# Optimization experiments

Hardware: AMD Instinct MI355X
Metric: run time of the kernel (lower is better)

The kernel has to match this reference:

```python
import jax, jax.numpy as jnp
import numpy as np

N = 200_000      # nodes
E = 6_400_000    # edges (avg degree 32)
ATT = 16         # scorer hidden dim
MAXD = 512       # mixer max_depth
C = 1.0          # curvature
EPS = 1e-15


def _mobius_add(a, b, c):
    # Mobius addition on the Poincare ball: a (+)_c b
    ab = jnp.sum(a * b, axis=-1, keepdims=True)
    aa = jnp.sum(a * a, axis=-1, keepdims=True)
    bb = jnp.sum(b * b, axis=-1, keepdims=True)
    num = (1.0 + 2.0 * c * ab + c * bb) * a + (1.0 - c * aa) * b
    den = 1.0 + 2.0 * c * ab + (c * c) * aa * bb
    return num / jnp.maximum(den, EPS)


def setup_inputs() -> dict:
    key = jax.random.key(0)
    ks = jax.random.split(key, 8)
    x = jax.random.normal(ks[0], (N, 2), dtype=jnp.float32)
    # keep nodes strictly inside the unit Poincare disk (|x| < 0.5)
    x = 0.5 * x / (1.0 + jnp.linalg.norm(x, axis=-1, keepdims=True))
    edge_index = jax.random.randint(ks[1], (2, E), 0, N, dtype=jnp.int32)
    depth = jax.random.randint(ks[2], (N,), 0, MAXD, dtype=jnp.int32)
    W1 = jax.random.normal(ks[3], (2, ATT), dtype=jnp.float32) * (1.0 / np.sqrt(2.0))
    b1 = jnp.zeros((ATT,), dtype=jnp.float32)
    W2 = jax.random.normal(ks[4], (ATT, 1), dtype=jnp.float32) * (1.0 / np.sqrt(ATT))
    eta = jnp.array(1.0, dtype=jnp.float32)
    depth_scale = 1.0 + 0.1 * jax.random.normal(ks[5], (MAXD, 1), dtype=jnp.float32)
    depth_theta = 0.1 * jax.random.normal(ks[6], (MAXD, 1), dtype=jnp.float32)
    return dict(x=x, edge_index=edge_index, depth=depth, W1=W1, b1=b1, W2=W2,
                eta=eta, depth_scale=depth_scale, depth_theta=depth_theta)


def reference(x, edge_index, depth, W1, b1, W2, eta, depth_scale, depth_theta):
    c = C
    sc = jnp.sqrt(jnp.asarray(c, dtype=x.dtype))
    row, col = edge_index[0], edge_index[1]
    xi = x[row]   # [E,2] target node of each edge
    xj = x[col]   # [E,2] source node of each edge

    # log_{xi}(xj): tangent vector at xi
    u = _mobius_add(-xi, xj, c)                                        # [E,2]
    un = jnp.maximum(jnp.linalg.norm(u, axis=-1, keepdims=True), EPS)  # [E,1]
    lam_i = 2.0 / jnp.maximum(1.0 - c * jnp.sum(xi * xi, axis=-1, keepdims=True), EPS)
    v = (2.0 / (sc * lam_i)) * jnp.arctanh(jnp.minimum(sc * un, 1.0 - 1e-5)) * (u / un)

    # tiny MLP attention score per edge
    h = jax.nn.gelu(v @ W1 + b1, approximate=False)   # [E,ATT]
    scores = (h @ W2)[:, 0]                           # [E]

    # segment softmax over edges grouped by target node `row`
    smax = jax.ops.segment_max(scores, row, num_segments=N)
    ex = jnp.exp(scores - smax[row])
    denom = jax.ops.segment_sum(ex, row, num_segments=N)
    alpha = ex / jnp.maximum(denom[row], 1e-15)       # [E]

    # weighted scatter-add of tangent vectors
    m = jax.ops.segment_sum(alpha[:, None] * v, row, num_segments=N)   # [N,2]

    # depth-gated rotation/scale in the tangent space (mixer)
    d = jnp.clip(depth, 0, MAXD - 1)
    k = depth_scale[d]            # [N,1]
    ang = depth_theta[d][:, 0]    # [N]
    ca, sa = jnp.cos(ang), jnp.sin(ang)
    m = k * jnp.stack([ca * m[:, 0] - sa * m[:, 1],
                       sa * m[:, 0] + ca * m[:, 1]], axis=-1)

    # exp_{x}(eta * m)
    w = eta * m
    wn = jnp.maximum(jnp.linalg.norm(w, axis=-1, keepdims=True), EPS)
    lam_x = 2.0 / jnp.maximum(1.0 - c * jnp.sum(x * x, axis=-1, keepdims=True), EPS)
    second = jnp.tanh(sc * lam_x * wn / 2.0) * (w / (sc * wn))
    return _mobius_add(x, second, c)
```

## Files before the change

### kernel.cpp

```cpp
#include <hip/hip_runtime.h>
#include <hip/hip_fp16.h>
#include <math.h>

#define EPSF 1e-15f
#define BSH  8
#define BSZ  (1 << BSH)
#define BMSK (BSZ - 1)
#define CAPB 9216
#define MAXNB 1024
#define AGG_T 1024
#define BIN_T 1024
#define LCH   6400

#define TBL   128
#define TW    129
#define VMIN  (-1.2f)
#define VH    (2.4f / 128.0f)
#define INVH  (128.0f / 2.4f)

__device__ __forceinline__ float fast_rcp(float x)  { return __builtin_amdgcn_rcpf(x); }
__device__ __forceinline__ float fast_rsq(float x)  { return __builtin_amdgcn_rsqf(x); }
__device__ __forceinline__ float fast_exp(float x)  { return __builtin_amdgcn_exp2f(x * 1.4426950408889634f); }

__device__ __forceinline__ unsigned int float_to_ordered(float f) {
    unsigned int u = __float_as_uint(f);
    return (u & 0x80000000u) ? ~u : (u | 0x80000000u);
}
__device__ __forceinline__ float ordered_to_float(unsigned int u) {
    u = (u & 0x80000000u) ? (u & 0x7FFFFFFFu) : ~u;
    return __uint_as_float(u);
}

__device__ __forceinline__ void edge_v_fast(float2 xi, float2 xj, float& vx, float& vy) {
    float ab = -(xi.x * xj.x + xi.y * xj.y);
    float aa = xi.x * xi.x + xi.y * xi.y;
    float bb = xj.x * xj.x + xj.y * xj.y;
    float f1 = 1.0f + 2.0f * ab + bb;
    float f2 = 1.0f - aa;
    float ux = f1 * (-xi.x) + f2 * xj.x;
    float uy = f1 * (-xi.y) + f2 * xj.y;
    float den = 1.0f + 2.0f * ab + aa * bb;
    float inv_den = fast_rcp(fmaxf(den, EPSF));
    ux *= inv_den; uy *= inv_den;
    float un2 = fmaxf(ux * ux + uy * uy, 1e-24f);
    float inv_un = fast_rsq(un2);
    float un = fminf(un2 * inv_un, 1.0f - 1e-5f);
    float t = 0.34657359027997264f * __builtin_amdgcn_logf((1.0f + un) * fast_rcp(1.0f - un));
    float s = fmaxf(f2, EPSF) * t * inv_un;
    vx = s * ux; vy = s * uy;
}

__device__ __forceinline__ void edge_v(float2 xi, float2 xj, float& vx, float& vy) {
    float ab = -(xi.x * xj.x + xi.y * xj.y);
    float aa = xi.x * xi.x + xi.y * xi.y;
    float bb = xj.x * xj.x + xj.y * xj.y;
    float f1 = 1.0f + 2.0f * ab + bb;
    float f2 = 1.0f - aa;
    float ux = f1 * (-xi.x) + f2 * xj.x;
    float uy = f1 * (-xi.y) + f2 * xj.y;
    float den = 1.0f + 2.0f * ab + aa * bb;
    float inv_den = 1.0f / fmaxf(den, EPSF);
    ux *= inv_den; uy *= inv_den;
    float un = fmaxf(sqrtf(ux * ux + uy * uy), EPSF);
    float t  = atanhf(fminf(un, 1.0f - 1e-5f));
    float s = fmaxf(f2, EPSF) * t / un;
    vx = s * ux; vy = s * uy;
}

__device__ __forceinline__ float edge_score(float vx, float vy,
                                            const float* __restrict__ W1,
                                            const float* __restrict__ b1,
                                            const float* __restrict__ W2) {
    float score = 0.0f;
#pragma unroll
    for (int k = 0; k < 16; ++k) {
        float z = fmaf(vx, W1[k], fmaf(vy, W1[16 + k], b1[k]));
        float g = 0.5f * z * (1.0f + erff(z * 0.70710678118654752f));
        score = fmaf(g, W2[k], score);
    }
    return score;
}

__device__ __forceinline__ float2 finalize_node(float2 xv, float mx, float my,
                                                int d, float eta,
                                                const float* __restrict__ dscale,
                                                const float* __restrict__ dtheta) {
    d = d < 0 ? 0 : (d > 511 ? 511 : d);
    float k   = dscale[d];
    float ang = dtheta[d];
    float ca = cosf(ang), sa = sinf(ang);
    float m0 = k * (ca * mx - sa * my);
    float m1 = k * (sa * mx + ca * my);

    float wx = eta * m0, wy = eta * m1;
    float wn = fmaxf(sqrtf(wx * wx + wy * wy), 1e-15f);

    float aa = xv.x * xv.x + xv.y * xv.y;
    float lam = 2.0f / fmaxf(1.0f - aa, 1e-15f);
    float fac = tanhf(lam * wn * 0.5f) / wn;
    float sx = fac * wx, sy = fac * wy;

    float ab = xv.x * sx + xv.y * sy;
    float bb = sx * sx + sy * sy;
    float n1 = 1.0f + 2.0f * ab + bb;
    float n2 = 1.0f - aa;
    float ox = n1 * xv.x + n2 * sx;
    float oy = n1 * xv.y + n2 * sy;
    float dd = 1.0f + 2.0f * ab + aa * bb;
    float inv = 1.0f / fmaxf(dd, 1e-15f);
    return make_float2(ox * inv, oy * inv);
}


__global__ void init_cursor(unsigned* __restrict__ cursor, int NB) {
    int b = blockIdx.x * blockDim.x + threadIdx.x;
    if (b < NB) cursor[b] = (unsigned)b * CAPB;
}

__global__ void build_score_table(const float* __restrict__ W1,
                                  const float* __restrict__ b1,
                                  const float* __restrict__ W2,
                                  float* __restrict__ tbl) {
    int i = blockIdx.x * blockDim.x + threadIdx.x;
    if (i >= TW * TW) return;
    int iy = i / TW, ix = i - iy * TW;
    float vx = VMIN + VH * (float)ix;
    float vy = VMIN + VH * (float)iy;
    tbl[i] = edge_score(vx, vy, W1, b1, W2);
}

__global__ __launch_bounds__(BIN_T)
void bin_edges(const int* __restrict__ ei,
               unsigned* __restrict__ cursor,
               unsigned* __restrict__ sorted,
               int E, int NB) {
    __shared__ unsigned bkrank[LCH];
    __shared__ unsigned payload[LCH];
    __shared__ unsigned sortedLoc[LCH];
    __shared__ unsigned gdst[LCH];
    __shared__ unsigned hist[MAXNB];
    __shared__ unsigned scanA[MAXNB];
    __shared__ unsigned loc[MAXNB];
    __shared__ unsigned gbase[MAXNB];

    int tid = threadIdx.x;
    int e0 = blockIdx.x * LCH;
    int cnt = min(E - e0, LCH);
    if (cnt <= 0) return;

    if (tid < MAXNB) hist[tid] = 0;
    __syncthreads();

    for (int idx = tid; idx < cnt; idx += BIN_T) {
        int r = ei[e0 + idx];
        int c = ei[E + e0 + idx];
        unsigned bk = (unsigned)r >> BSH;
        unsigned rank = atomicAdd(&hist[bk], 1u);
        bkrank[idx] = (bk << 14) | rank;
        payload[idx] = ((unsigned)(r & BMSK) << 24) | (unsigned)c;
    }
    __syncthreads();

    unsigned h = (tid < MAXNB) ? hist[tid] : 0u;
    if (tid < MAXNB) scanA[tid] = h;
    __syncthreads();
#pragma unroll
    for (int step = 1; step < MAXNB; step <<= 1) {
        unsigned v = 0u;
        if (tid < MAXNB) {
            v = scanA[tid];
            if (tid >= step) v += scanA[tid - step];
        }
        __syncthreads();
        if (tid < MAXNB) scanA[tid] = v;
        __syncthreads();
    }
    if (tid < MAXNB) {
        loc[tid] = scanA[tid] - h;
        gbase[tid] = h ? atomicAdd(&cursor[tid], h) : 0u;
    }
    __syncthreads();

    for (int idx = tid; idx < cnt; idx += BIN_T) {
        unsigned v = bkrank[idx];
        unsigned bk = v >> 14;
        unsigned rank = v & 0x3FFFu;
        unsigned pos = loc[bk] + rank;
        sortedLoc[pos] = payload[idx];
        unsigned g = gbase[bk] + rank;
        gdst[pos] = (g < (bk + 1u) * CAPB) ? g : 0xFFFFFFFFu;
    }
    __syncthreads();

    for (int idx = tid; idx < cnt; idx += BIN_T) {
        unsigned g = gdst[idx];
        if (g != 0xFFFFFFFFu) sorted[g] = sortedLoc[idx];
    }
}

__global__ __launch_bounds__(AGG_T, 8)
void aggregate(const float2* __restrict__ x,
               const unsigned* __restrict__ cursor,
               const unsigned* __restrict__ sorted,
               const int* __restrict__ depth,
               const float* __restrict__ tbl,
               const float* __restrict__ etaPtr,
               const float* __restrict__ dscale,
               const float* __restrict__ dtheta,
               float2* __restrict__ out, int N) {
    __shared__ float2 xr[BSZ];
    __shared__ unsigned stashA[CAPB];
    __shared__ unsigned stashV[CAPB];
    __shared__ unsigned nmax[BSZ];
    __shared__ unsigned long long accP[BSZ];

    int b = blockIdx.x;
    int tid = threadIdx.x;
    int nb0 = b << BSH;
    int nodeCnt = min(BSZ, N - nb0);
    if (tid < BSZ) {
        nmax[tid] = 0u;
        accP[tid] = 0ull;
        if (tid < nodeCnt) xr[tid] = x[nb0 + tid];
    }
    __syncthreads();

    unsigned basep = (unsigned)b * CAPB;
    unsigned cnt = cursor[b] - basep;
    cnt = cnt > (unsigned)CAPB ? (unsigned)CAPB : cnt;

    for (unsigned i = tid; i < cnt; i += AGG_T) {
        unsigned u = sorted[basep + i];
        int rl = (int)(u >> 24);
        int c  = (int)(u & 0xFFFFFFu);
        float2 xi = xr[rl];
        float2 xj = x[c];
        float vx, vy;
        edge_v_fast(xi, xj, vx, vy);

        float tx = fminf(fmaxf((vx - VMIN) * INVH, 0.0f), 127.999f);
        float ty = fminf(fmaxf((vy - VMIN) * INVH, 0.0f), 127.999f);
        int ix = (int)tx, iy = (int)ty;
        float fx = tx - (float)ix, fy = ty - (float)iy;
        const float* row = tbl + iy * TW + ix;
        float s00 = row[0], s01 = row[1];
        float s10 = row[TW], s11 = row[TW + 1];
        float sA = fmaf(fx, s01 - s00, s00);
        float sB = fmaf(fx, s11 - s10, s10);
        float score = fmaf(fy, sB - sA, sA);

        __half hs = __float2half_rn(score);
        float sq = __half2float(hs);
        unsigned short s16 = *(unsigned short*)&hs;
        __half2 h2 = __floats2half2_rn(vx, vy);
        stashA[i] = ((unsigned)rl << 16) | (unsigned)s16;
        stashV[i] = *(unsigned*)&h2;
        atomicMax(&nmax[rl], float_to_ordered(sq));
    }
    __syncthreads();

    for (unsigned i = tid; i < cnt; i += AGG_T) {
        unsigned a = stashA[i];
        int rl = (int)(a >> 16);
        unsigned short s16 = (unsigned short)(a & 0xFFFFu);
        __half hs = *(__half*)&s16;
        float s = __half2float(hs);
        float mxs = ordered_to_float(nmax[rl]);
        float ex = fast_exp(s - mxs);
        unsigned vv = stashV[i];
        __half2 h2 = *(__half2*)&vv;
        float2 v2 = __half22float2(h2);
        unsigned e0 = __float2uint_rn(ex * 16384.0f);
        unsigned e1 = __float2uint_rn(ex * (v2.x + 2.0f) * 0.25f * 16384.0f);
        unsigned e2 = __float2uint_rn(ex * (v2.y + 2.0f) * 0.25f * 16384.0f);
        unsigned long long pk = (unsigned long long)e0
                              | ((unsigned long long)e1 << 21)
                              | ((unsigned long long)e2 << 42);
        atomicAdd(&accP[rl], pk);
    }
    __syncthreads();

    if (tid >= nodeCnt) return;
    unsigned long long w = accP[tid];
    float F0 = (float)(unsigned int)(w & 0x1FFFFFull);
    float F1 = (float)(unsigned int)((w >> 21) & 0x1FFFFFull);
    float F2 = (float)(unsigned int)(w >> 42);
    float mx = 0.0f, my = 0.0f;
    if (F0 > 0.0f) {
        float inv = 1.0f / F0;
        mx = 4.0f * F1 * inv - 2.0f;
        my = 4.0f * F2 * inv - 2.0f;
    }
    int i = nb0 + tid;
    out[i] = finalize_node(xr[tid], mx, my, depth[i], etaPtr[0], dscale, dtheta);
}


__global__ void init_kernel(unsigned int* __restrict__ smax,
                            unsigned long long* __restrict__ maccP, int N) {
    int i = blockIdx.x * blockDim.x + threadIdx.x;
    if (i < N) {
        smax[i] = float_to_ordered(-INFINITY);
        maccP[i] = 0ull;
    }
}

__global__ void pass1_score_max(const float2* __restrict__ x,
                                const int* __restrict__ ei,
                                const float* __restrict__ W1,
                                const float* __restrict__ b1,
                                const float* __restrict__ W2,
                                unsigned int* __restrict__ smax, int E) {
    int e = blockIdx.x * blockDim.x + threadIdx.x;
    if (e >= E) return;
    int r = ei[e];
    int c = ei[E + e];
    float vx, vy;
    edge_v(x[r], x[c], vx, vy);
    float score = edge_score(vx, vy, W1, b1, W2);
    atomicMax(&smax[r], float_to_ordered(score));
}

#define PK_SCALE 16384.0f

__global__ void pass2_accum(const float2* __restrict__ x,
                            const int* __restrict__ ei,
                            const float* __restrict__ W1,
                            const float* __restrict__ b1,
                            const float* __restrict__ W2,
                            const unsigned int* __restrict__ smax,
                            unsigned long long* __restrict__ maccP, int E) {
    int e = blockIdx.x * blockDim.x + threadIdx.x;
    if (e >= E) return;
    int r = ei[e];
    int c = ei[E + e];
    float vx, vy;
    edge_v(x[r], x[c], vx, vy);
    float score = edge_score(vx, vy, W1, b1, W2);
    float mx = ordered_to_float(smax[r]);
    float ex = expf(score - mx);
    unsigned e0 = __float2uint_rn(ex * PK_SCALE);
    unsigned e1 = __float2uint_rn(ex * (vx + 2.0f) * 0.25f * PK_SCALE);
    unsigned e2 = __float2uint_rn(ex * (vy + 2.0f) * 0.25f * PK_SCALE);
    unsigned long long pk = (unsigned long long)e0
                          | ((unsigned long long)e1 << 21)
                          | ((unsigned long long)e2 << 42);
    atomicAdd(&maccP[r], pk);
}

__global__ void pass3_finalize(const float2* __restrict__ x,
                               const int* __restrict__ depth,
                               const unsigned long long* __restrict__ maccP,
                               const float* __restrict__ etaPtr,
                               const float* __restrict__ dscale,
                               const float* __restrict__ dtheta,
                               float2* __restrict__ out, int N) {
    int i = blockIdx.x * blockDim.x + threadIdx.x;
    if (i >= N) return;
    unsigned long long w = maccP[i];
    float F0 = (float)(unsigned int)(w & 0x1FFFFFull);
    float F1 = (float)(unsigned int)((w >> 21) & 0x1FFFFFull);
    float F2 = (float)(unsigned int)(w >> 42);
    float mx = 0.0f, my = 0.0f;
    if (F0 > 0.0f) {
        float inv = 1.0f / F0;
        mx = 4.0f * F1 * inv - 2.0f;
        my = 4.0f * F2 * inv - 2.0f;
    }
    out[i] = finalize_node(x[i], mx, my, depth[i], etaPtr[0], dscale, dtheta);
}


extern "C" void kernel_launch(void* const* d_in, const int* in_sizes, int n_in,
                              void* d_out, int out_size, void* d_ws, size_t ws_size,
                              hipStream_t stream) {
    const float2* x   = (const float2*)d_in[0];
    const int* ei     = (const int*)d_in[1];
    const int* depth  = (const int*)d_in[2];
    const float* W1   = (const float*)d_in[3];
    const float* b1   = (const float*)d_in[4];
    const float* W2   = (const float*)d_in[5];
    const float* eta  = (const float*)d_in[6];
    const float* dsc  = (const float*)d_in[7];
    const float* dth  = (const float*)d_in[8];
    float2* out = (float2*)d_out;

    int N = in_sizes[0] / 2;
    int E = in_sizes[1] / 2;
    int NB = (N + BSZ - 1) >> BSH;

    const int B = 256;
    size_t sortedBytes = (size_t)NB * CAPB * 4;
    size_t need = 4096 + sortedBytes + (size_t)TW * TW * 4;
    if (NB <= MAXNB && ws_size >= need) {
        unsigned* cursor = (unsigned*)d_ws;
        unsigned* sorted = (unsigned*)((char*)d_ws + 4096);
        float* tbl = (float*)((char*)d_ws + 4096 + sortedBytes);
        int binG = (E + LCH - 1) / LCH;
        init_cursor<<<(NB + B - 1) / B, B, 0, stream>>>(cursor, NB);
        build_score_table<<<(TW * TW + B - 1) / B, B, 0, stream>>>(W1, b1, W2, tbl);
        bin_edges<<<binG, BIN_T, 0, stream>>>(ei, cursor, sorted, E, NB);
        aggregate<<<NB, AGG_T, 0, stream>>>(x, cursor, sorted, depth, tbl,
                                            eta, dsc, dth, out, N);
    } else {
        unsigned long long* maccP = (unsigned long long*)d_ws;
        unsigned int* smax = (unsigned int*)(maccP + N);
        init_kernel<<<(N + B - 1) / B, B, 0, stream>>>(smax, maccP, N);
        pass1_score_max<<<(E + B - 1) / B, B, 0, stream>>>(x, ei, W1, b1, W2, smax, E);
        pass2_accum<<<(E + B - 1) / B, B, 0, stream>>>(x, ei, W1, b1, W2, smax, maccP, E);
        pass3_finalize<<<(N + B - 1) / B, B, 0, stream>>>(x, depth, maccP, eta, dsc, dth, out, N);
    }
}
```

Baseline: 195.3 us.

## Keep per-edge stash in registers and batch-load edge gathers in aggregate

Replaces the two 9216-entry LDS stash arrays with per-thread register arrays covering a fixed 9 slots per thread. Each thread first issues all of its sorted-edge loads and then all of its x[c] gathers, so the gathers are in flight together rather than serialized with compute. Dropping about 72KB of LDS per block should allow more blocks per CU. The cost is higher register pressure from the fully unrolled loops, and inactive slots still read sorted and x[0].

```diff
diff --git a/kernel.cpp b/kernel.cpp
--- a/kernel.cpp
+++ b/kernel.cpp
@@ -9,6 +9,7 @@
 #define CAPB 9216
 #define MAXNB 1024
 #define AGG_T 1024
+#define KSL   9
 #define BIN_T 1024
 #define LCH   6400
 
@@ -209,8 +210,6 @@
                const float* __restrict__ dtheta,
                float2* __restrict__ out, int N) {
     __shared__ float2 xr[BSZ];
-    __shared__ unsigned stashA[CAPB];
-    __shared__ unsigned stashV[CAPB];
     __shared__ unsigned nmax[BSZ];
     __shared__ unsigned long long accP[BSZ];
 
@@ -228,15 +227,34 @@
     unsigned basep = (unsigned)b * CAPB;
     unsigned cnt = cursor[b] - basep;
     cnt = cnt > (unsigned)CAPB ? (unsigned)CAPB : cnt;
-
-    for (unsigned i = tid; i < cnt; i += AGG_T) {
-        unsigned u = sorted[basep + i];
-        int rl = (int)(u >> 24);
-        int c  = (int)(u & 0xFFFFFFu);
-        float2 xi = xr[rl];
-        float2 xj = x[c];
+    const unsigned* __restrict__ sb = sorted + basep;
+
+    unsigned u[KSL];
+#pragma unroll
+    for (int k = 0; k < KSL; ++k) {
+        u[k] = sb[(unsigned)tid + (unsigned)(k * AGG_T)];
+    }
+
+    int rl[KSL];
+    float2 xj[KSL];
+#pragma unroll
+    for (int k = 0; k < KSL; ++k) {
+        unsigned i = (unsigned)tid + (unsigned)(k * AGG_T);
+        bool act = i < cnt;
+        rl[k] = (int)(u[k] >> 24);
+        int c = act ? (int)(u[k] & 0xFFFFFFu) : 0;
+        xj[k] = x[c];
+    }
+
+    unsigned pkA[KSL];
+    unsigned pkV[KSL];
+#pragma unroll
+    for (int k = 0; k < KSL; ++k) {
+        unsigned i = (unsigned)tid + (unsigned)(k * AGG_T);
+        bool act = i < cnt;
+        float2 xi = xr[rl[k]];
         float vx, vy;
-        edge_v_fast(xi, xj, vx, vy);
+        edge_v_fast(xi, xj[k], vx, vy);
 
         float tx = fminf(fmaxf((vx - VMIN) * INVH, 0.0f), 127.999f);
         float ty = fminf(fmaxf((vy - VMIN) * INVH, 0.0f), 127.999f);
@@ -253,22 +271,23 @@
         float sq = __half2float(hs);
         unsigned short s16 = *(unsigned short*)&hs;
         __half2 h2 = __floats2half2_rn(vx, vy);
-        stashA[i] = ((unsigned)rl << 16) | (unsigned)s16;
-        stashV[i] = *(unsigned*)&h2;
-        atomicMax(&nmax[rl], float_to_ordered(sq));
-    }
-    __syncthreads();
-
-    for (unsigned i = tid; i < cnt; i += AGG_T) {
-        unsigned a = stashA[i];
-        int rl = (int)(a >> 16);
-        unsigned short s16 = (unsigned short)(a & 0xFFFFu);
+        pkA[k] = ((unsigned)rl[k] << 16) | (unsigned)s16;
+        pkV[k] = *(unsigned*)&h2;
+        if (act) atomicMax(&nmax[rl[k]], float_to_ordered(sq));
+    }
+    __syncthreads();
+
+#pragma unroll
+    for (int k = 0; k < KSL; ++k) {
+        unsigned i = (unsigned)tid + (unsigned)(k * AGG_T);
+        if (i >= cnt) continue;
+        int rlk = (int)(pkA[k] >> 16);
+        unsigned short s16 = (unsigned short)(pkA[k] & 0xFFFFu);
         __half hs = *(__half*)&s16;
         float s = __half2float(hs);
-        float mxs = ordered_to_float(nmax[rl]);
+        float mxs = ordered_to_float(nmax[rlk]);
         float ex = fast_exp(s - mxs);
-        unsigned vv = stashV[i];
-        __half2 h2 = *(__half2*)&vv;
+        __half2 h2 = *(__half2*)&pkV[k];
         float2 v2 = __half22float2(h2);
         unsigned e0 = __float2uint_rn(ex * 16384.0f);
         unsigned e1 = __float2uint_rn(ex * (v2.x + 2.0f) * 0.25f * 16384.0f);
@@ -276,7 +295,7 @@
         unsigned long long pk = (unsigned long long)e0
                               | ((unsigned long long)e1 << 21)
                               | ((unsigned long long)e2 << 42);
-        atomicAdd(&accP[rl], pk);
+        atomicAdd(&accP[rlk], pk);
     }
     __syncthreads();
 
```

Result: no change. 193.0 us (-1.2%).

## Replace edge binning with global-max softmax and direct global atomics

Applied to the files above, without the earlier changes.

Drops the bucket-sort and per-node segment max. The softmax is stabilised with the global maximum of the score lookup table, which is mathematically equivalent. Each edge then atomically adds fixed-point weighted sums straight into per-node global accumulators, with the table staged in LDS. This removes the bin_edges pass and the sorted buffer traffic, but adds 6.4M random global 64-bit and 32-bit atomics, and it risks fixed-point underflow when a node's scores sit far below the global max.

```diff
diff --git a/kernel.cpp b/kernel.cpp
--- a/kernel.cpp
+++ b/kernel.cpp
@@ -3,20 +3,19 @@
 #include <math.h>
 
 #define EPSF 1e-15f
-#define BSH  8
-#define BSZ  (1 << BSH)
-#define BMSK (BSZ - 1)
-#define CAPB 9216
-#define MAXNB 1024
-#define AGG_T 1024
-#define BIN_T 1024
-#define LCH   6400
 
 #define TBL   128
 #define TW    129
+#define TWSZ  (TW * TW)
+#define TW4   ((TWSZ) / 4)
 #define VMIN  (-1.2f)
 #define VH    (2.4f / 128.0f)
 #define INVH  (128.0f / 2.4f)
+
+#define ACC_SCALE 16777216.0f
+
+#define FUS_T 1024
+#define FPT   4
 
 __device__ __forceinline__ float fast_rcp(float x)  { return __builtin_amdgcn_rcpf(x); }
 __device__ __forceinline__ float fast_rsq(float x)  { return __builtin_amdgcn_rsqf(x); }
@@ -112,187 +111,124 @@
 }
 
 
-__global__ void init_cursor(unsigned* __restrict__ cursor, int NB) {
-    int b = blockIdx.x * blockDim.x + threadIdx.x;
-    if (b < NB) cursor[b] = (unsigned)b * CAPB;
-}
-
 __global__ void build_score_table(const float* __restrict__ W1,
                                   const float* __restrict__ b1,
                                   const float* __restrict__ W2,
-                                  float* __restrict__ tbl) {
+                                  float* __restrict__ tbl,
+                                  unsigned* __restrict__ tblMaxSlot) {
     int i = blockIdx.x * blockDim.x + threadIdx.x;
-    if (i >= TW * TW) return;
+    if (i >= TWSZ) return;
     int iy = i / TW, ix = i - iy * TW;
     float vx = VMIN + VH * (float)ix;
     float vy = VMIN + VH * (float)iy;
-    tbl[i] = edge_score(vx, vy, W1, b1, W2);
-}
-
-__global__ __launch_bounds__(BIN_T)
-void bin_edges(const int* __restrict__ ei,
-               unsigned* __restrict__ cursor,
-               unsigned* __restrict__ sorted,
-               int E, int NB) {
-    __shared__ unsigned bkrank[LCH];
-    __shared__ unsigned payload[LCH];
-    __shared__ unsigned sortedLoc[LCH];
-    __shared__ unsigned gdst[LCH];
-    __shared__ unsigned hist[MAXNB];
-    __shared__ unsigned scanA[MAXNB];
-    __shared__ unsigned loc[MAXNB];
-    __shared__ unsigned gbase[MAXNB];
+    float v = edge_score(vx, vy, W1, b1, W2);
+    tbl[i] = v;
+    atomicMax(tblMaxSlot, float_to_ordered(v));
+}
+
+__global__ __launch_bounds__(FUS_T, 8)
+void fused_edges(const float2* __restrict__ x,
+                 const int* __restrict__ ei,
+                 const float* __restrict__ tbl,
+                 const unsigned* __restrict__ tblMaxSlot,
+                 unsigned long long* __restrict__ accP,
+                 unsigned* __restrict__ accE,
+                 int E) {
+    __shared__ __align__(16) float tl[TWSZ];
 
     int tid = threadIdx.x;
-    int e0 = blockIdx.x * LCH;
-    int cnt = min(E - e0, LCH);
-    if (cnt <= 0) return;
-
-    if (tid < MAXNB) hist[tid] = 0;
+    int base = (blockIdx.x * FUS_T + tid) * FPT;
+
+    int rr[FPT], cc[FPT];
+    if (base + FPT <= E) {
+        int4 r4 = *(const int4*)(ei + base);
+        int4 c4 = *(const int4*)(ei + E + base);
+        rr[0] = r4.x; rr[1] = r4.y; rr[2] = r4.z; rr[3] = r4.w;
+        cc[0] = c4.x; cc[1] = c4.y; cc[2] = c4.z; cc[3] = c4.w;
+    } else {
+#pragma unroll
+        for (int k = 0; k < FPT; ++k) {
+            int e = base + k;
+            rr[k] = (e < E) ? ei[e] : 0;
+            cc[k] = (e < E) ? ei[E + e] : 0;
+        }
+    }
+    __builtin_amdgcn_sched_barrier(0);
+
+    {
+        const float4* t4 = (const float4*)tbl;
+        float4* tl4 = (float4*)tl;
+#pragma unroll
+        for (int k = 0; k < 4; ++k) {
+            int i = tid + k * FUS_T;
+            tl4[i] = t4[i];
+        }
+        int i5 = tid + 4 * FUS_T;
+        if (i5 < TW4) tl4[i5] = t4[i5];
+        if (tid == 0) tl[TWSZ - 1] = tbl[TWSZ - 1];
+    }
+    float tblMax = ordered_to_float(*tblMaxSlot);
+    if (!(tblMax > -1e30f && tblMax < 1e30f)) tblMax = 0.0f;
     __syncthreads();
 
-    for (int idx = tid; idx < cnt; idx += BIN_T) {
-        int r = ei[e0 + idx];
-        int c = ei[E + e0 + idx];
-        unsigned bk = (unsigned)r >> BSH;
-        unsigned rank = atomicAdd(&hist[bk], 1u);
-        bkrank[idx] = (bk << 14) | rank;
-        payload[idx] = ((unsigned)(r & BMSK) << 24) | (unsigned)c;
-    }
-    __syncthreads();
-
-    unsigned h = (tid < MAXNB) ? hist[tid] : 0u;
-    if (tid < MAXNB) scanA[tid] = h;
-    __syncthreads();
-#pragma unroll
-    for (int step = 1; step < MAXNB; step <<= 1) {
-        unsigned v = 0u;
-        if (tid < MAXNB) {
-            v = scanA[tid];
-            if (tid >= step) v += scanA[tid - step];
-        }
-        __syncthreads();
-        if (tid < MAXNB) scanA[tid] = v;
-        __syncthreads();
-    }
-    if (tid < MAXNB) {
-        loc[tid] = scanA[tid] - h;
-        gbase[tid] = h ? atomicAdd(&cursor[tid], h) : 0u;
-    }
-    __syncthreads();
-
-    for (int idx = tid; idx < cnt; idx += BIN_T) {
-        unsigned v = bkrank[idx];
-        unsigned bk = v >> 14;
-        unsigned rank = v & 0x3FFFu;
-        unsigned pos = loc[bk] + rank;
-        sortedLoc[pos] = payload[idx];
-        unsigned g = gbase[bk] + rank;
-        gdst[pos] = (g < (bk + 1u) * CAPB) ? g : 0xFFFFFFFFu;
-    }
-    __syncthreads();
-
-    for (int idx = tid; idx < cnt; idx += BIN_T) {
-        unsigned g = gdst[idx];
-        if (g != 0xFFFFFFFFu) sorted[g] = sortedLoc[idx];
-    }
-}
-
-__global__ __launch_bounds__(AGG_T, 8)
-void aggregate(const float2* __restrict__ x,
-               const unsigned* __restrict__ cursor,
-               const unsigned* __restrict__ sorted,
-               const int* __restrict__ depth,
-               const float* __restrict__ tbl,
-               const float* __restrict__ etaPtr,
-               const float* __restrict__ dscale,
-               const float* __restrict__ dtheta,
-               float2* __restrict__ out, int N) {
-    __shared__ float2 xr[BSZ];
-    __shared__ unsigned stashA[CAPB];
-    __shared__ unsigned stashV[CAPB];
-    __shared__ unsigned nmax[BSZ];
-    __shared__ unsigned long long accP[BSZ];
-
-    int b = blockIdx.x;
-    int tid = threadIdx.x;
-    int nb0 = b << BSH;
-    int nodeCnt = min(BSZ, N - nb0);
-    if (tid < BSZ) {
-        nmax[tid] = 0u;
-        accP[tid] = 0ull;
-        if (tid < nodeCnt) xr[tid] = x[nb0 + tid];
-    }
-    __syncthreads();
-
-    unsigned basep = (unsigned)b * CAPB;
-    unsigned cnt = cursor[b] - basep;
-    cnt = cnt > (unsigned)CAPB ? (unsigned)CAPB : cnt;
-
-    for (unsigned i = tid; i < cnt; i += AGG_T) {
-        unsigned u = sorted[basep + i];
-        int rl = (int)(u >> 24);
-        int c  = (int)(u & 0xFFFFFFu);
-        float2 xi = xr[rl];
-        float2 xj = x[c];
+    if (base >= E) return;
+
+    float2 xi[FPT], xj[FPT];
+#pragma unroll
+    for (int k = 0; k < FPT; ++k) {
+        bool act = (base + k) < E;
+        xi[k] = x[act ? rr[k] : 0];
+        xj[k] = x[act ? cc[k] : 0];
+    }
+    __builtin_amdgcn_sched_barrier(0);
+
+#pragma unroll
+    for (int k = 0; k < FPT; ++k) {
+        if ((base + k) >= E) continue;
         float vx, vy;
-        edge_v_fast(xi, xj, vx, vy);
+        edge_v_fast(xi[k], xj[k], vx, vy);
 
         float tx = fminf(fmaxf((vx - VMIN) * INVH, 0.0f), 127.999f);
         float ty = fminf(fmaxf((vy - VMIN) * INVH, 0.0f), 127.999f);
         int ix = (int)tx, iy = (int)ty;
         float fx = tx - (float)ix, fy = ty - (float)iy;
-        const float* row = tbl + iy * TW + ix;
+        const float* row = tl + iy * TW + ix;
         float s00 = row[0], s01 = row[1];
         float s10 = row[TW], s11 = row[TW + 1];
         float sA = fmaf(fx, s01 - s00, s00);
         float sB = fmaf(fx, s11 - s10, s10);
         float score = fmaf(fy, sB - sA, sA);
 
-        __half hs = __float2half_rn(score);
-        float sq = __half2float(hs);
-        unsigned short s16 = *(unsigned short*)&hs;
-        __half2 h2 = __floats2half2_rn(vx, vy);
-        stashA[i] = ((unsigned)rl << 16) | (unsigned)s16;
-        stashV[i] = *(unsigned*)&h2;
-        atomicMax(&nmax[rl], float_to_ordered(sq));
-    }
-    __syncthreads();
-
-    for (unsigned i = tid; i < cnt; i += AGG_T) {
-        unsigned a = stashA[i];
-        int rl = (int)(a >> 16);
-        unsigned short s16 = (unsigned short)(a & 0xFFFFu);
-        __half hs = *(__half*)&s16;
-        float s = __half2float(hs);
-        float mxs = ordered_to_float(nmax[rl]);
-        float ex = fast_exp(s - mxs);
-        unsigned vv = stashV[i];
-        __half2 h2 = *(__half2*)&vv;
-        float2 v2 = __half22float2(h2);
-        unsigned e0 = __float2uint_rn(ex * 16384.0f);
-        unsigned e1 = __float2uint_rn(ex * (v2.x + 2.0f) * 0.25f * 16384.0f);
-        unsigned e2 = __float2uint_rn(ex * (v2.y + 2.0f) * 0.25f * 16384.0f);
-        unsigned long long pk = (unsigned long long)e0
-                              | ((unsigned long long)e1 << 21)
-                              | ((unsigned long long)e2 << 42);
-        atomicAdd(&accP[rl], pk);
-    }
-    __syncthreads();
-
-    if (tid >= nodeCnt) return;
-    unsigned long long w = accP[tid];
-    float F0 = (float)(unsigned int)(w & 0x1FFFFFull);
-    float F1 = (float)(unsigned int)((w >> 21) & 0x1FFFFFull);
-    float F2 = (float)(unsigned int)(w >> 42);
+        float ex = fast_exp(score - tblMax);
+        unsigned e0 = __float2uint_rn(ex * ACC_SCALE);
+        unsigned e1 = __float2uint_rn(ex * (vx + 2.0f) * 0.25f * ACC_SCALE);
+        unsigned e2 = __float2uint_rn(ex * (vy + 2.0f) * 0.25f * ACC_SCALE);
+        atomicAdd(&accP[rr[k]], (unsigned long long)e1 | ((unsigned long long)e2 << 32));
+        atomicAdd(&accE[rr[k]], e0);
+    }
+}
+
+__global__ void finalize_nodes(const float2* __restrict__ x,
+                               const int* __restrict__ depth,
+                               const unsigned long long* __restrict__ accP,
+                               const unsigned* __restrict__ accE,
+                               const float* __restrict__ etaPtr,
+                               const float* __restrict__ dscale,
+                               const float* __restrict__ dtheta,
+                               float2* __restrict__ out, int N) {
+    int i = blockIdx.x * blockDim.x + threadIdx.x;
+    if (i >= N) return;
+    unsigned long long w = accP[i];
+    float F0 = (float)accE[i];
+    float F1 = (float)(unsigned int)(w & 0xFFFFFFFFull);
+    float F2 = (float)(unsigned int)(w >> 32);
     float mx = 0.0f, my = 0.0f;
     if (F0 > 0.0f) {
         float inv = 1.0f / F0;
         mx = 4.0f * F1 * inv - 2.0f;
         my = 4.0f * F2 * inv - 2.0f;
     }
-    int i = nb0 + tid;
-    out[i] = finalize_node(xr[tid], mx, my, depth[i], etaPtr[0], dscale, dtheta);
+    out[i] = finalize_node(x[i], mx, my, depth[i], etaPtr[0], dscale, dtheta);
 }
 
 
@@ -387,21 +323,24 @@
 
     int N = in_sizes[0] / 2;
     int E = in_sizes[1] / 2;
-    int NB = (N + BSZ - 1) >> BSH;
 
     const int B = 256;
-    size_t sortedBytes = (size_t)NB * CAPB * 4;
-    size_t need = 4096 + sortedBytes + (size_t)TW * TW * 4;
-    if (NB <= MAXNB && ws_size >= need) {
-        unsigned* cursor = (unsigned*)d_ws;
-        unsigned* sorted = (unsigned*)((char*)d_ws + 4096);
-        float* tbl = (float*)((char*)d_ws + 4096 + sortedBytes);
-        int binG = (E + LCH - 1) / LCH;
-        init_cursor<<<(NB + B - 1) / B, B, 0, stream>>>(cursor, NB);
-        build_score_table<<<(TW * TW + B - 1) / B, B, 0, stream>>>(W1, b1, W2, tbl);
-        bin_edges<<<binG, BIN_T, 0, stream>>>(ei, cursor, sorted, E, NB);
-        aggregate<<<NB, AGG_T, 0, stream>>>(x, cursor, sorted, depth, tbl,
-                                            eta, dsc, dth, out, N);
+    size_t offAccP = 64;
+    size_t offAccE = offAccP + (size_t)N * 8;
+    size_t offTbl  = offAccE + (size_t)N * 4;
+    size_t need    = offTbl + (size_t)TWSZ * 4;
+    if (ws_size >= need && (N % 4) == 0) {
+        unsigned* tblMaxSlot = (unsigned*)d_ws;
+        unsigned long long* accP = (unsigned long long*)((char*)d_ws + offAccP);
+        unsigned* accE = (unsigned*)((char*)d_ws + offAccE);
+        float* tbl = (float*)((char*)d_ws + offTbl);
+
+        hipMemsetAsync(d_ws, 0, offTbl, stream);
+        build_score_table<<<(TWSZ + B - 1) / B, B, 0, stream>>>(W1, b1, W2, tbl, tblMaxSlot);
+        int fusG = (E + FUS_T * FPT - 1) / (FUS_T * FPT);
+        fused_edges<<<fusG, FUS_T, 0, stream>>>(x, ei, tbl, tblMaxSlot, accP, accE, E);
+        finalize_nodes<<<(N + B - 1) / B, B, 0, stream>>>(x, depth, accP, accE,
+                                                          eta, dsc, dth, out, N);
     } else {
         unsigned long long* maccP = (unsigned long long*)d_ws;
         unsigned int* smax = (unsigned int*)(maccP + N);
```

New measurement: 639.9 us. 3.28x slower.
